# Kernel optimization log

Measured on AMD Instinct MI355X. Metric: run time of the kernel, lower is better.

The kernel has to match this reference:

```python
import jax, jax.numpy as jnp
import numpy as np


def _sobel_mag(x_bchw):
    # per-channel Sobel gradient magnitude, then mean over channels -> [B,1,H,W]
    B, C, H, W = x_bchw.shape
    kx = jnp.array([[-1, 0, 1], [-2, 0, 2], [-1, 0, 1]], dtype=x_bchw.dtype).reshape(1, 1, 3, 3)
    ky = jnp.array([[-1, -2, -1], [0, 0, 0], [1, 2, 1]], dtype=x_bchw.dtype).reshape(1, 1, 3, 3)
    xf = x_bchw.reshape(B * C, 1, H, W)
    dn = ('NCHW', 'OIHW', 'NCHW')
    gx = jax.lax.conv_general_dilated(xf, kx, (1, 1), 'SAME', dimension_numbers=dn)
    gy = jax.lax.conv_general_dilated(xf, ky, (1, 1), 'SAME', dimension_numbers=dn)
    mag = jnp.sqrt(gx * gx + gy * gy + 1e-8).reshape(B, C, H, W)
    return mag.mean(axis=1, keepdims=True)


def _bi_wkv(w, u, k, v):
    # Bidirectional WKV (Vision-RWKV):
    # y_t = (sum_{i!=t} exp(k_i - (|t-i|-1)*w) v_i + exp(u+k_t) v_t)
    #     / (sum_{i!=t} exp(k_i - (|t-i|-1)*w)     + exp(u+k_t))
    # w,u: [C];  k,v: [B,T,C]. Numerically stable prefix scans in both directions.
    B, T, C = k.shape
    kt = jnp.transpose(k, (1, 0, 2))  # [T,B,C]
    vt = jnp.transpose(v, (1, 0, 2))

    def scan_dir(ks, vs):
        def step(carry, kv):
            a, b, pp = carry  # running num, den at log-offset pp (exclusive prefix)
            kk, vv = kv
            out = (a, b, pp)
            ww = pp - w  # decay one step
            p = jnp.maximum(ww, kk)
            e1 = jnp.exp(ww - p)
            e2 = jnp.exp(kk - p)
            return (e1 * a + e2 * vv, e1 * b + e2, p), out
        init = (jnp.zeros((B, C), k.dtype), jnp.zeros((B, C), k.dtype),
                jnp.full((B, C), -1e38, k.dtype))
        _, (a, b, pp) = jax.lax.scan(step, init, (ks, vs))
        return a, b, pp

    af, bf, pf = scan_dir(kt, vt)                       # contributions i < t
    ab, bb, pb = scan_dir(kt[::-1], vt[::-1])           # contributions i > t
    ab, bb, pb = ab[::-1], bb[::-1], pb[::-1]

    ps = u + kt                                         # self term exponent
    m = jnp.maximum(jnp.maximum(pf, pb), ps)
    ef = jnp.exp(pf - m)
    eb = jnp.exp(pb - m)
    es = jnp.exp(ps - m)
    num = af * ef + ab * eb + es * vt
    den = bf * ef + bb * eb + es
    return jnp.transpose(num / den, (1, 0, 2))  # [B,T,C]


def setup_inputs() -> dict:
    key = jax.random.key(0)
    ks = jax.random.split(key, 8)
    B, H, W, C = 8, 64, 64, 256
    T = H * W
    s = 1.0 / np.sqrt(C)
    return {
        'x': jax.random.normal(ks[0], (B, T, C), jnp.float32),
        'Wk': jax.random.normal(ks[1], (C, C), jnp.float32) * s,
        'Wv': jax.random.normal(ks[2], (C, C), jnp.float32) * s,
        'Wr': jax.random.normal(ks[3], (C, C), jnp.float32) * s,
        'Wo': jax.random.normal(ks[4], (C, C), jnp.float32) * s,
        'spatial_decay': jax.random.uniform(ks[5], (C,), jnp.float32, 0.5, 1.5),
        'spatial_first': jax.random.uniform(ks[6], (C,), jnp.float32, 0.5, 1.5),
        'H': H,
        'W': W,
    }


def reference(x, Wk, Wv, Wr, Wo, spatial_decay, spatial_first, H, W):
    B, T, C = x.shape
    k = x @ Wk.T
    v = x @ Wv.T
    r = x @ Wr.T
    sr = jax.nn.sigmoid(r)
    # edge gate
    x_hw = jnp.transpose(x, (0, 2, 1)).reshape(B, C, H, W)
    edge_g = jax.nn.sigmoid(_sobel_mag(x_hw)).reshape(B, 1, T)
    sr = sr + jnp.transpose(edge_g, (0, 2, 1))
    # bi-directional WKV with w,u scaled by 1/T (as in forward)
    xwkv = _bi_wkv(spatial_decay / T, spatial_first / T, k, v)
    return (sr * xwkv) @ Wo.T
```

## Files before the change

### kernel.cpp

```cpp
#include <hip/hip_runtime.h>
#include <hip/hip_bf16.h>

#define TB 8
#define TT 4096
#define TC 256
#define NC2 128
#define CL2 32

#define K2 512
#define BM 128
#define BN 128
#define BK 64

typedef _Float16 half8 __attribute__((ext_vector_type(8)));
typedef _Float16 half2v __attribute__((ext_vector_type(2)));
typedef float floatx4 __attribute__((ext_vector_type(4)));

#define GLDS16(g, l) __builtin_amdgcn_global_load_lds( \
    (const __attribute__((address_space(1))) void*)(g), \
    (__attribute__((address_space(3))) void*)(l), 16, 0, 0)

__global__ __launch_bounds__(256) void sobconv(
    const float* __restrict__ x, _Float16* __restrict__ X2,
    float* __restrict__ edge)
{
    int t = blockIdx.x & (TT - 1);
    int b = blockIdx.x >> 12;
    int h = t >> 6, w = t & 63;
    int c = threadIdx.x;

    float n[3][3];
    #pragma unroll
    for (int dh = 0; dh < 3; dh++) {
        int hh = h + dh - 1;
        #pragma unroll
        for (int dw = 0; dw < 3; dw++) {
            int ww = w + dw - 1;
            float val = 0.f;
            if (hh >= 0 && hh < 64 && ww >= 0 && ww < 64)
                val = x[((size_t)(b * TT + (hh << 6) + ww)) * TC + c];
            n[dh][dw] = val;
        }
    }
    float xc = n[1][1];
    _Float16 hi = (_Float16)xc;
    _Float16 lo = (_Float16)(xc - (float)hi);
    half2v p; p.x = hi; p.y = lo;
    *(half2v*)(X2 + ((size_t)(b * TT + t)) * K2 + 2 * c) = p;

    float gx = (n[0][2] - n[0][0]) + 2.f * (n[1][2] - n[1][0]) + (n[2][2] - n[2][0]);
    float gy = (n[2][0] + 2.f * n[2][1] + n[2][2]) - (n[0][0] + 2.f * n[0][1] + n[0][2]);
    float mag = sqrtf(gx * gx + gy * gy + 1e-8f);

    #pragma unroll
    for (int off = 32; off > 0; off >>= 1) mag += __shfl_down(mag, off, 64);
    __shared__ float part[4];
    if ((threadIdx.x & 63) == 0) part[threadIdx.x >> 6] = mag;
    __syncthreads();
    if (threadIdx.x == 0) {
        float s = part[0] + part[1] + part[2] + part[3];
        edge[blockIdx.x] = 1.f / (1.f + __expf(-s * (1.f / 256.f)));
    }
}

__global__ __launch_bounds__(256) void convert_w(
    const float* __restrict__ Wk, const float* __restrict__ Wv,
    const float* __restrict__ Wr, const float* __restrict__ Wo,
    _Float16* __restrict__ W2, _Float16* __restrict__ Wo2)
{
    int t = blockIdx.x * 256 + threadIdx.x;
    int wsel = t >> 16;
    int i = t & 65535;
    const float* src = (wsel == 0) ? Wk : (wsel == 1) ? Wv : (wsel == 2) ? Wr : Wo;
    _Float16* dst = (wsel < 3) ? (W2 + (size_t)wsel * TC * K2) : Wo2;
    _Float16 h = (_Float16)src[i];
    half2v p; p.x = h; p.y = h;
    *(half2v*)(dst + 2 * (size_t)i) = p;
}

__global__ __launch_bounds__(256) void gemm_f16(
    const _Float16* __restrict__ A2,
    const _Float16* __restrict__ W0, const _Float16* __restrict__ W1,
    const _Float16* __restrict__ W2p,
    void* __restrict__ C0, void* __restrict__ C1, void* __restrict__ C2,
    int ops)
{
    __shared__ __align__(16) char smem[32768];
    _Float16* As = (_Float16*)smem;
    _Float16* Bs = (_Float16*)(smem + 16384);

    int by = blockIdx.y;
    int wsel = by >> 1;
    const _Float16* W = (wsel == 0) ? W0 : (wsel == 1) ? W1 : W2p;
    void* Cc          = (wsel == 0) ? C0 : (wsel == 1) ? C1 : C2;
    int col0 = (by & 1) * BN;
    int row0 = blockIdx.x * BM;
    int op = (ops >> (2 * wsel)) & 3;

    int tid = threadIdx.x;
    int lane = tid & 63;
    int wv = tid >> 6;
    int qm = (wv >> 1) * 64;
    int qn = (wv & 1) * 64;

    const _Float16* Ag = A2 + (size_t)row0 * K2;
    const _Float16* Bg = W + (size_t)col0 * K2;

    floatx4 acc[4][4];
    #pragma unroll
    for (int i = 0; i < 4; i++)
        #pragma unroll
        for (int j = 0; j < 4; j++)
            acc[i][j] = (floatx4){0.f, 0.f, 0.f, 0.f};

    for (int kb = 0; kb < K2; kb += BK) {
        __syncthreads();
        #pragma unroll
        for (int i = 0; i < 4; i++) {
            int seg = i * 256 + tid;
            int row = seg >> 3;
            int s = seg & 7;
            int sg = s ^ (row & 7);
            GLDS16(Ag + (size_t)row * K2 + kb + sg * 8, &As[seg * 8]);
            GLDS16(Bg + (size_t)row * K2 + kb + sg * 8, &Bs[seg * 8]);
        }
        __syncthreads();
        #pragma unroll
        for (int kk = 0; kk < 2; kk++) {
            int sl = kk * 4 + (lane >> 4);
            half8 a[4], b[4];
            #pragma unroll
            for (int i = 0; i < 4; i++) {
                int ra = qm + i * 16 + (lane & 15);
                a[i] = *(const half8*)&As[ra * BK + ((sl ^ (ra & 7)) * 8)];
                int rb = qn + i * 16 + (lane & 15);
                b[i] = *(const half8*)&Bs[rb * BK + ((sl ^ (rb & 7)) * 8)];
            }
            #pragma unroll
            for (int i = 0; i < 4; i++)
                #pragma unroll
                for (int j = 0; j < 4; j++)
                    acc[i][j] = __builtin_amdgcn_mfma_f32_16x16x32_f16(
                        a[i], b[j], acc[i][j], 0, 0, 0);
        }
    }

    int mr0 = (lane >> 4) * 4;
    int nc = lane & 15;
    if (op == 2) {
        __syncthreads();
        ushort* tile = (ushort*)smem;
        #pragma unroll
        for (int i = 0; i < 4; i++)
            #pragma unroll
            for (int r = 0; r < 4; r++) {
                int ml = qm + i * 16 + mr0 + r;
                #pragma unroll
                for (int j = 0; j < 4; j++) {
                    int nl = qn + j * 16 + nc;
                    float vv = __expf(acc[i][j][r]);
                    _Float16 hh = (_Float16)vv;
                    tile[ml * 128 + (nl ^ (((ml >> 2) & 3) << 4))] = *(ushort*)&hh;
                }
            }
        __syncthreads();
        _Float16* Ch = (_Float16*)Cc;
        #pragma unroll
        for (int k = 0; k < 8; k++) {
            int seg = k * 256 + tid;
            int tr = seg >> 4;
            int ts = seg & 15;
            int ts2 = ts ^ (((tr >> 2) & 3) << 1);
            float4 val = *(const float4*)&tile[tr * 128 + ts2 * 8];
            ((float4*)(Ch + (size_t)(row0 + tr) * TC + col0))[ts] = val;
        }
    } else {
        float* Cf = (float*)Cc;
        #pragma unroll
        for (int i = 0; i < 4; i++) {
            #pragma unroll
            for (int r = 0; r < 4; r++) {
                int m = row0 + qm + i * 16 + mr0 + r;
                float* crow = Cf + (size_t)m * TC + col0 + qn;
                #pragma unroll
                for (int j = 0; j < 4; j++) {
                    float vvv = acc[i][j][r];
                    if (op == 1) vvv = 1.f / (1.f + __expf(-vvv));
                    crow[j * 16 + nc] = vvv;
                }
            }
        }
    }
}

__global__ __launch_bounds__(256) void wkv_chunk_sums(
    const _Float16* __restrict__ ekp, const float* __restrict__ vp,
    const float* __restrict__ decay,
    float* __restrict__ SaF, float* __restrict__ SbF,
    float* __restrict__ RaB, float* __restrict__ RbB)
{
    int tid = blockIdx.x * 256 + threadIdx.x;
    int c = tid & 255;
    int j = (tid >> 8) & (NC2 - 1);
    int b = tid >> 15;
    float w = decay[c] * (1.f / (float)TT);
    float d = __expf(-w);
    size_t base = ((size_t)(b * TT + j * CL2)) * TC + c;
    float Sa = 0.f, Sb = 0.f, Ra = 0.f, Rb = 0.f, pw = 1.f;
    #pragma unroll
    for (int i = 0; i < CL2; i++) {
        float ek = (float)ekp[base + (size_t)i * TC];
        float vv = vp[base + (size_t)i * TC];
        float ekv = ek * vv;
        Sa = fmaf(d, Sa, ekv);
        Sb = fmaf(d, Sb, ek);
        Ra = fmaf(pw, ekv, Ra);
        Rb = fmaf(pw, ek, Rb);
        pw *= d;
    }
    int idx = (b * NC2 + j) * TC + c;
    SaF[idx] = Sa; SbF[idx] = Sb; RaB[idx] = Ra; RbB[idx] = Rb;
}

__global__ __launch_bounds__(256) void wkv_carries(
    const float* __restrict__ SaF, const float* __restrict__ SbF,
    const float* __restrict__ RaB, const float* __restrict__ RbB,
    const float* __restrict__ decay,
    float* __restrict__ CfA, float* __restrict__ CfB,
    float* __restrict__ CbA, float* __restrict__ CbB)
{
    int gw = (blockIdx.x * 256 + threadIdx.x) >> 6;
    int lane = threadIdx.x & 63;
    int c = gw & 255, b = gw >> 8;
    float w = decay[c] * (1.f / (float)TT);
    float D = __expf(-(float)CL2 * w);
    int base = b * NC2 * TC + c;
    int j0 = 2 * lane, j1 = 2 * lane + 1;
    int r0 = NC2 - 1 - j0, r1 = NC2 - 2 - j0;

    float sa0 = SaF[base + j0 * TC], sa1 = SaF[base + j1 * TC];
    float sb0 = SbF[base + j0 * TC], sb1 = SbF[base + j1 * TC];
    float qa0 = RaB[base + r0 * TC], qa1 = RaB[base + r1 * TC];
    float qb0 = RbB[base + r0 * TC], qb1 = RbB[base + r1 * TC];

    float pa = fmaf(D, sa0, sa1), pb = fmaf(D, sb0, sb1);
    float ra = fmaf(D, qa0, qa1), rb = fmaf(D, qb0, qb1);

    float dp = D * D;
    #pragma unroll
    for (int off = 1; off < 64; off <<= 1) {
        float ta = __shfl_up(pa, off, 64);
        float tb = __shfl_up(pb, off, 64);
        float ua = __shfl_up(ra, off, 64);
        float ub = __shfl_up(rb, off, 64);
        if (lane >= off) {
            pa = fmaf(dp, ta, pa); pb = fmaf(dp, tb, pb);
            ra = fmaf(dp, ua, ra); rb = fmaf(dp, ub, rb);
        }
        dp = dp * dp;
    }
    float ppa = __shfl_up(pa, 1, 64);
    float ppb = __shfl_up(pb, 1, 64);
    float pra = __shfl_up(ra, 1, 64);
    float prb = __shfl_up(rb, 1, 64);
    if (lane == 0) { ppa = 0.f; ppb = 0.f; pra = 0.f; prb = 0.f; }

    CfA[base + j0 * TC] = ppa;
    CfA[base + j1 * TC] = fmaf(D, ppa, sa0);
    CfB[base + j0 * TC] = ppb;
    CfB[base + j1 * TC] = fmaf(D, ppb, sb0);
    CbA[base + r0 * TC] = pra;
    CbA[base + r1 * TC] = fmaf(D, pra, qa0);
    CbB[base + r0 * TC] = prb;
    CbB[base + r1 * TC] = fmaf(D, prb, qb0);
}

__global__ __launch_bounds__(256) void wkv_combine(
    const _Float16* __restrict__ ekp, const float* __restrict__ vp,
    const float* __restrict__ srp, const float* __restrict__ edgep,
    const float* __restrict__ decay, const float* __restrict__ first,
    const float* __restrict__ CfA, const float* __restrict__ CfB,
    const float* __restrict__ CbA, const float* __restrict__ CbB,
    _Float16* __restrict__ Y2)
{
    int bid = blockIdx.x;
    int j = bid & (NC2 - 1);
    int b = bid >> 7;
    int c = threadIdx.x;

    float w = decay[c] * (1.f / (float)TT);
    float d = __expf(-w);
    float eu = __expf(first[c] * (1.f / (float)TT));
    int cidx = (b * NC2 + j) * TC + c;
    size_t base = ((size_t)(b * TT + j * CL2)) * TC + c;

    float abArr[CL2], bbArr[CL2];
    float ab = CbA[cidx], bb = CbB[cidx];
    #pragma unroll
    for (int i = CL2 - 1; i >= 0; i--) {
        float ek = (float)ekp[base + (size_t)i * TC];
        float vv = vp[base + (size_t)i * TC];
        abArr[i] = ab; bbArr[i] = bb;
        ab = fmaf(d, ab, ek * vv);
        bb = fmaf(d, bb, ek);
    }
    float af = CfA[cidx], bf = CfB[cidx];
    #pragma unroll
    for (int i = 0; i < CL2; i++) {
        size_t idx = base + (size_t)i * TC;
        float ek = (float)ekp[idx];
        float vv = vp[idx];
        float srv = srp[idx];
        float es = ek * eu;
        float num = af + abArr[i] + es * vv;
        float den = bf + bbArr[i] + es;
        float ev = edgep[b * TT + j * CL2 + i];
        float yv = (srv + ev) * (num / den);
        _Float16 yh = (_Float16)yv;
        _Float16 yl = (_Float16)(yv - (float)yh);
        half2v p; p.x = yh; p.y = yl;
        size_t m = (size_t)(b * TT + j * CL2 + i);
        *(half2v*)(Y2 + m * K2 + 2 * c) = p;
        af = fmaf(d, af, ek * vv);
        bf = fmaf(d, bf, ek);
    }
}

extern "C" void kernel_launch(void* const* d_in, const int* in_sizes, int n_in,
                              void* d_out, int out_size, void* d_ws, size_t ws_size,
                              hipStream_t stream)
{
    const float* x      = (const float*)d_in[0];
    const float* Wk     = (const float*)d_in[1];
    const float* Wv     = (const float*)d_in[2];
    const float* Wr     = (const float*)d_in[3];
    const float* Wo     = (const float*)d_in[4];
    const float* sdecay = (const float*)d_in[5];
    const float* sfirst = (const float*)d_in[6];
    float* out = (float*)d_out;

    char* ws = (char*)d_ws;
    size_t off = 0;
    const size_t MB32 = (size_t)TB * TT * TC * sizeof(float);
    const size_t XH   = (size_t)TB * TT * K2 * sizeof(_Float16);
    _Float16* X2   = (_Float16*)(ws + off); off += XH;
    _Float16* ekh  = (_Float16*)(ws + off); off += MB32 / 2;
    float* vbuf  = (float*)(ws + off); off += MB32;
    float* srbuf = (float*)(ws + off); off += MB32;
    _Float16* W2  = (_Float16*)(ws + off); off += (size_t)3 * TC * K2 * sizeof(_Float16);
    _Float16* Wo2 = (_Float16*)(ws + off); off += (size_t)TC * K2 * sizeof(_Float16);
    float* edge  = (float*)(ws + off); off += (size_t)TB * TT * sizeof(float);
    const size_t CHB = (size_t)TB * NC2 * TC * sizeof(float);
    float* SaF = (float*)(ws + off); off += CHB;
    float* SbF = (float*)(ws + off); off += CHB;
    float* RaB = (float*)(ws + off); off += CHB;
    float* RbB = (float*)(ws + off); off += CHB;
    float* CfA = (float*)(ws + off); off += CHB;
    float* CfB = (float*)(ws + off); off += CHB;
    float* CbA = (float*)(ws + off); off += CHB;
    float* CbB = (float*)(ws + off); off += CHB;

    const int MBLK = (TB * TT) / BM;

    convert_w<<<(4 * TC * TC) / 256, 256, 0, stream>>>(Wk, Wv, Wr, Wo, W2, Wo2);
    sobconv<<<TB * TT, 256, 0, stream>>>(x, X2, edge);

    int ops1 = (2 << 0) | (0 << 2) | (1 << 4);
    gemm_f16<<<dim3(MBLK, 6), 256, 0, stream>>>(
        X2, W2, W2 + (size_t)TC * K2, W2 + (size_t)2 * TC * K2,
        ekh, vbuf, srbuf, ops1);

    wkv_chunk_sums<<<(TB * NC2 * TC) / 256, 256, 0, stream>>>(
        ekh, vbuf, sdecay, SaF, SbF, RaB, RbB);
    wkv_carries<<<(TB * TC * 64) / 256, 256, 0, stream>>>(
        SaF, SbF, RaB, RbB, sdecay, CfA, CfB, CbA, CbB);
    wkv_combine<<<TB * NC2, 256, 0, stream>>>(
        ekh, vbuf, srbuf, edge, sdecay, sfirst, CfA, CfB, CbA, CbB, X2);

    gemm_f16<<<dim3(MBLK, 2), 256, 0, stream>>>(
        X2, Wo2, Wo2, Wo2, out, out, out, 0);
}
```

Measured before the change: 222.5 us.

## Split hi/lo activations into separate planes and widen GEMM tile to full N

Stores the fp16 hi and lo parts of activations in two separate arrays instead of interleaving them along a doubled K. The GEMM now loads the weight tile once and issues two MFMAs per (hi, lo) pair, with a 128x256 block tile (BK=32), which removes the duplicated weight storage and halves the B-operand traffic. The weight conversion is also folded into the Sobel prep kernel, saving a launch. The exp-to-fp16 epilogue now writes directly to global instead of staging through LDS, so its stores are less coalesced. The larger accumulator array raises register pressure.

```diff
diff --git a/kernel.cpp b/kernel.cpp
--- a/kernel.cpp
+++ b/kernel.cpp
@@ -7,23 +7,35 @@
 #define NC2 128
 #define CL2 32
 
-#define K2 512
-#define BM 128
-#define BN 128
-#define BK 64
-
 typedef _Float16 half8 __attribute__((ext_vector_type(8)));
-typedef _Float16 half2v __attribute__((ext_vector_type(2)));
+typedef _Float16 half4v __attribute__((ext_vector_type(4)));
 typedef float floatx4 __attribute__((ext_vector_type(4)));
 
 #define GLDS16(g, l) __builtin_amdgcn_global_load_lds( \
     (const __attribute__((address_space(1))) void*)(g), \
     (__attribute__((address_space(3))) void*)(l), 16, 0, 0)
 
-__global__ __launch_bounds__(256) void sobconv(
-    const float* __restrict__ x, _Float16* __restrict__ X2,
-    float* __restrict__ edge)
-{
+__global__ __launch_bounds__(256) void prep(
+    const float* __restrict__ x,
+    const float* __restrict__ Wk, const float* __restrict__ Wv,
+    const float* __restrict__ Wr, const float* __restrict__ Wo,
+    _Float16* __restrict__ Xh, _Float16* __restrict__ Xl,
+    _Float16* __restrict__ Wf, float* __restrict__ edge)
+{
+    if (blockIdx.x >= TB * TT) {
+        int t4 = (blockIdx.x - TB * TT) * 256 + threadIdx.x;
+        int f = t4 * 4;
+        int wsel = f >> 16;
+        int i = f & 65535;
+        const float* src = (wsel == 0) ? Wk : (wsel == 1) ? Wv :
+                           (wsel == 2) ? Wr : Wo;
+        float4 v = *(const float4*)(src + i);
+        half4v h;
+        h.x = (_Float16)v.x; h.y = (_Float16)v.y;
+        h.z = (_Float16)v.z; h.w = (_Float16)v.w;
+        *(half4v*)(Wf + (size_t)wsel * 65536 + i) = h;
+        return;
+    }
     int t = blockIdx.x & (TT - 1);
     int b = blockIdx.x >> 12;
     int h = t >> 6, w = t & 63;
@@ -45,8 +57,9 @@
     float xc = n[1][1];
     _Float16 hi = (_Float16)xc;
     _Float16 lo = (_Float16)(xc - (float)hi);
-    half2v p; p.x = hi; p.y = lo;
-    *(half2v*)(X2 + ((size_t)(b * TT + t)) * K2 + 2 * c) = p;
+    size_t mi = (size_t)(b * TT + t) * TC + c;
+    Xh[mi] = hi;
+    Xl[mi] = lo;
 
     float gx = (n[0][2] - n[0][0]) + 2.f * (n[1][2] - n[1][0]) + (n[2][2] - n[2][0]);
     float gy = (n[2][0] + 2.f * n[2][1] + n[2][2]) - (n[0][0] + 2.f * n[0][1] + n[0][2]);
@@ -63,131 +76,106 @@
     }
 }
 
-__global__ __launch_bounds__(256) void convert_w(
-    const float* __restrict__ Wk, const float* __restrict__ Wv,
-    const float* __restrict__ Wr, const float* __restrict__ Wo,
-    _Float16* __restrict__ W2, _Float16* __restrict__ Wo2)
-{
-    int t = blockIdx.x * 256 + threadIdx.x;
-    int wsel = t >> 16;
-    int i = t & 65535;
-    const float* src = (wsel == 0) ? Wk : (wsel == 1) ? Wv : (wsel == 2) ? Wr : Wo;
-    _Float16* dst = (wsel < 3) ? (W2 + (size_t)wsel * TC * K2) : Wo2;
-    _Float16 h = (_Float16)src[i];
-    half2v p; p.x = h; p.y = h;
-    *(half2v*)(dst + 2 * (size_t)i) = p;
-}
-
-__global__ __launch_bounds__(256) void gemm_f16(
-    const _Float16* __restrict__ A2,
+__global__ __launch_bounds__(256, 2) void gemm_split(
+    const _Float16* __restrict__ Ah_g, const _Float16* __restrict__ Al_g,
     const _Float16* __restrict__ W0, const _Float16* __restrict__ W1,
     const _Float16* __restrict__ W2p,
     void* __restrict__ C0, void* __restrict__ C1, void* __restrict__ C2,
     int ops)
 {
-    __shared__ __align__(16) char smem[32768];
-    _Float16* As = (_Float16*)smem;
-    _Float16* Bs = (_Float16*)(smem + 16384);
-
-    int by = blockIdx.y;
-    int wsel = by >> 1;
+    __shared__ __align__(16) _Float16 smem[16384];
+    _Float16* Ah = smem;
+    _Float16* Al = smem + 4096;
+    _Float16* Bs = smem + 8192;
+
+    int wsel = blockIdx.y;
     const _Float16* W = (wsel == 0) ? W0 : (wsel == 1) ? W1 : W2p;
     void* Cc          = (wsel == 0) ? C0 : (wsel == 1) ? C1 : C2;
-    int col0 = (by & 1) * BN;
-    int row0 = blockIdx.x * BM;
     int op = (ops >> (2 * wsel)) & 3;
+    int row0 = blockIdx.x * 128;
 
     int tid = threadIdx.x;
     int lane = tid & 63;
     int wv = tid >> 6;
     int qm = (wv >> 1) * 64;
-    int qn = (wv & 1) * 64;
-
-    const _Float16* Ag = A2 + (size_t)row0 * K2;
-    const _Float16* Bg = W + (size_t)col0 * K2;
-
-    floatx4 acc[4][4];
+    int qn = (wv & 1) * 128;
+
+    floatx4 acc[4][8];
     #pragma unroll
     for (int i = 0; i < 4; i++)
         #pragma unroll
-        for (int j = 0; j < 4; j++)
+        for (int j = 0; j < 8; j++)
             acc[i][j] = (floatx4){0.f, 0.f, 0.f, 0.f};
 
-    for (int kb = 0; kb < K2; kb += BK) {
+    for (int kb = 0; kb < 256; kb += 32) {
         __syncthreads();
         #pragma unroll
+        for (int r = 0; r < 2; r++) {
+            int q = r * 256 + tid;
+            int row = q >> 2;
+            int s = q & 3;
+            int g = (s - row - (row >> 2)) & 3;
+            size_t goff = (size_t)(row0 + row) * TC + kb + g * 8;
+            GLDS16(Ah_g + goff, &Ah[q * 8]);
+            GLDS16(Al_g + goff, &Al[q * 8]);
+        }
+        #pragma unroll
+        for (int r = 0; r < 4; r++) {
+            int q = r * 256 + tid;
+            int row = q >> 2;
+            int s = q & 3;
+            int g = (s - row - (row >> 2)) & 3;
+            GLDS16(W + (size_t)row * TC + kb + g * 8, &Bs[q * 8]);
+        }
+        __syncthreads();
+        int sl = lane >> 4;
+        half8 ah[4], al[4], b[8];
+        #pragma unroll
         for (int i = 0; i < 4; i++) {
-            int seg = i * 256 + tid;
-            int row = seg >> 3;
-            int s = seg & 7;
-            int sg = s ^ (row & 7);
-            GLDS16(Ag + (size_t)row * K2 + kb + sg * 8, &As[seg * 8]);
-            GLDS16(Bg + (size_t)row * K2 + kb + sg * 8, &Bs[seg * 8]);
-        }
-        __syncthreads();
-        #pragma unroll
-        for (int kk = 0; kk < 2; kk++) {
-            int sl = kk * 4 + (lane >> 4);
-            half8 a[4], b[4];
+            int ra = qm + i * 16 + (lane & 15);
+            int sa = (sl + ra + (ra >> 2)) & 3;
+            ah[i] = *(const half8*)&Ah[ra * 32 + sa * 8];
+            al[i] = *(const half8*)&Al[ra * 32 + sa * 8];
+        }
+        #pragma unroll
+        for (int j = 0; j < 8; j++) {
+            int rb = qn + j * 16 + (lane & 15);
+            int sb = (sl + rb + (rb >> 2)) & 3;
+            b[j] = *(const half8*)&Bs[rb * 32 + sb * 8];
+        }
+        #pragma unroll
+        for (int i = 0; i < 4; i++)
             #pragma unroll
-            for (int i = 0; i < 4; i++) {
-                int ra = qm + i * 16 + (lane & 15);
-                a[i] = *(const half8*)&As[ra * BK + ((sl ^ (ra & 7)) * 8)];
-                int rb = qn + i * 16 + (lane & 15);
-                b[i] = *(const half8*)&Bs[rb * BK + ((sl ^ (rb & 7)) * 8)];
+            for (int j = 0; j < 8; j++) {
+                acc[i][j] = __builtin_amdgcn_mfma_f32_16x16x32_f16(
+                    ah[i], b[j], acc[i][j], 0, 0, 0);
+                acc[i][j] = __builtin_amdgcn_mfma_f32_16x16x32_f16(
+                    al[i], b[j], acc[i][j], 0, 0, 0);
             }
-            #pragma unroll
-            for (int i = 0; i < 4; i++)
-                #pragma unroll
-                for (int j = 0; j < 4; j++)
-                    acc[i][j] = __builtin_amdgcn_mfma_f32_16x16x32_f16(
-                        a[i], b[j], acc[i][j], 0, 0, 0);
-        }
     }
 
     int mr0 = (lane >> 4) * 4;
     int nc = lane & 15;
-    if (op == 2) {
-        __syncthreads();
-        ushort* tile = (ushort*)smem;
-        #pragma unroll
-        for (int i = 0; i < 4; i++)
-            #pragma unroll
-            for (int r = 0; r < 4; r++) {
-                int ml = qm + i * 16 + mr0 + r;
+    #pragma unroll
+    for (int i = 0; i < 4; i++) {
+        #pragma unroll
+        for (int r = 0; r < 4; r++) {
+            int m = row0 + qm + i * 16 + mr0 + r;
+            if (op == 2) {
+                _Float16* crow = (_Float16*)Cc + (size_t)m * TC + qn + nc;
                 #pragma unroll
-                for (int j = 0; j < 4; j++) {
-                    int nl = qn + j * 16 + nc;
-                    float vv = __expf(acc[i][j][r]);
-                    _Float16 hh = (_Float16)vv;
-                    tile[ml * 128 + (nl ^ (((ml >> 2) & 3) << 4))] = *(ushort*)&hh;
-                }
-            }
-        __syncthreads();
-        _Float16* Ch = (_Float16*)Cc;
-        #pragma unroll
-        for (int k = 0; k < 8; k++) {
-            int seg = k * 256 + tid;
-            int tr = seg >> 4;
-            int ts = seg & 15;
-            int ts2 = ts ^ (((tr >> 2) & 3) << 1);
-            float4 val = *(const float4*)&tile[tr * 128 + ts2 * 8];
-            ((float4*)(Ch + (size_t)(row0 + tr) * TC + col0))[ts] = val;
-        }
-    } else {
-        float* Cf = (float*)Cc;
-        #pragma unroll
-        for (int i = 0; i < 4; i++) {
-            #pragma unroll
-            for (int r = 0; r < 4; r++) {
-                int m = row0 + qm + i * 16 + mr0 + r;
-                float* crow = Cf + (size_t)m * TC + col0 + qn;
+                for (int j = 0; j < 8; j++)
+                    crow[j * 16] = (_Float16)__expf(acc[i][j][r]);
+            } else if (op == 1) {
+                float* crow = (float*)Cc + (size_t)m * TC + qn + nc;
                 #pragma unroll
-                for (int j = 0; j < 4; j++) {
-                    float vvv = acc[i][j][r];
-                    if (op == 1) vvv = 1.f / (1.f + __expf(-vvv));
-                    crow[j * 16 + nc] = vvv;
-                }
+                for (int j = 0; j < 8; j++)
+                    crow[j * 16] = 1.f / (1.f + __expf(-acc[i][j][r]));
+            } else {
+                float* crow = (float*)Cc + (size_t)m * TC + qn + nc;
+                #pragma unroll
+                for (int j = 0; j < 8; j++)
+                    crow[j * 16] = acc[i][j][r];
             }
         }
     }
@@ -281,7 +269,7 @@
     const float* __restrict__ decay, const float* __restrict__ first,
     const float* __restrict__ CfA, const float* __restrict__ CfB,
     const float* __restrict__ CbA, const float* __restrict__ CbB,
-    _Float16* __restrict__ Y2)
+    _Float16* __restrict__ Yh, _Float16* __restrict__ Yl)
 {
     int bid = blockIdx.x;
     int j = bid & (NC2 - 1);
@@ -318,9 +306,8 @@
         float yv = (srv + ev) * (num / den);
         _Float16 yh = (_Float16)yv;
         _Float16 yl = (_Float16)(yv - (float)yh);
-        half2v p; p.x = yh; p.y = yl;
-        size_t m = (size_t)(b * TT + j * CL2 + i);
-        *(half2v*)(Y2 + m * K2 + 2 * c) = p;
+        Yh[idx] = yh;
+        Yl[idx] = yl;
         af = fmaf(d, af, ek * vv);
         bf = fmaf(d, bf, ek);
     }
@@ -341,14 +328,13 @@
 
     char* ws = (char*)d_ws;
     size_t off = 0;
-    const size_t MB32 = (size_t)TB * TT * TC * sizeof(float);
-    const size_t XH   = (size_t)TB * TT * K2 * sizeof(_Float16);
-    _Float16* X2   = (_Float16*)(ws + off); off += XH;
-    _Float16* ekh  = (_Float16*)(ws + off); off += MB32 / 2;
-    float* vbuf  = (float*)(ws + off); off += MB32;
-    float* srbuf = (float*)(ws + off); off += MB32;
-    _Float16* W2  = (_Float16*)(ws + off); off += (size_t)3 * TC * K2 * sizeof(_Float16);
-    _Float16* Wo2 = (_Float16*)(ws + off); off += (size_t)TC * K2 * sizeof(_Float16);
+    const size_t PH = (size_t)TB * TT * TC * sizeof(_Float16);
+    _Float16* Xh  = (_Float16*)(ws + off); off += PH;
+    _Float16* Xl  = (_Float16*)(ws + off); off += PH;
+    _Float16* ekh = (_Float16*)(ws + off); off += PH;
+    float* vbuf  = (float*)(ws + off); off += 2 * PH;
+    float* srbuf = (float*)(ws + off); off += 2 * PH;
+    _Float16* Wf = (_Float16*)(ws + off); off += (size_t)4 * TC * TC * sizeof(_Float16);
     float* edge  = (float*)(ws + off); off += (size_t)TB * TT * sizeof(float);
     const size_t CHB = (size_t)TB * NC2 * TC * sizeof(float);
     float* SaF = (float*)(ws + off); off += CHB;
@@ -360,23 +346,24 @@
     float* CbA = (float*)(ws + off); off += CHB;
     float* CbB = (float*)(ws + off); off += CHB;
 
-    const int MBLK = (TB * TT) / BM;
-
-    convert_w<<<(4 * TC * TC) / 256, 256, 0, stream>>>(Wk, Wv, Wr, Wo, W2, Wo2);
-    sobconv<<<TB * TT, 256, 0, stream>>>(x, X2, edge);
-
-    int ops1 = (2 << 0) | (0 << 2) | (1 << 4);
-    gemm_f16<<<dim3(MBLK, 6), 256, 0, stream>>>(
-        X2, W2, W2 + (size_t)TC * K2, W2 + (size_t)2 * TC * K2,
-        ekh, vbuf, srbuf, ops1);
+    _Float16* WfK = Wf;
+    _Float16* WfV = Wf + (size_t)TC * TC;
+    _Float16* WfR = Wf + (size_t)2 * TC * TC;
+    _Float16* WfO = Wf + (size_t)3 * TC * TC;
+
+    prep<<<TB * TT + 256, 256, 0, stream>>>(x, Wk, Wv, Wr, Wo, Xh, Xl, Wf, edge);
+
+    int ops1 = 2 | (0 << 2) | (1 << 4);
+    gemm_split<<<dim3((TB * TT) / 128, 3), 256, 0, stream>>>(
+        Xh, Xl, WfK, WfV, WfR, ekh, vbuf, srbuf, ops1);
 
     wkv_chunk_sums<<<(TB * NC2 * TC) / 256, 256, 0, stream>>>(
         ekh, vbuf, sdecay, SaF, SbF, RaB, RbB);
     wkv_carries<<<(TB * TC * 64) / 256, 256, 0, stream>>>(
         SaF, SbF, RaB, RbB, sdecay, CfA, CfB, CbA, CbB);
     wkv_combine<<<TB * NC2, 256, 0, stream>>>(
-        ekh, vbuf, srbuf, edge, sdecay, sfirst, CfA, CfB, CbA, CbB, X2);
-
-    gemm_f16<<<dim3(MBLK, 2), 256, 0, stream>>>(
-        X2, Wo2, Wo2, Wo2, out, out, out, 0);
-}
+        ekh, vbuf, srbuf, edge, sdecay, sfirst, CfA, CfB, CbA, CbB, Xh, Xl);
+
+    gemm_split<<<dim3((TB * TT) / 128, 1), 256, 0, stream>>>(
+        Xh, Xl, WfO, WfO, WfO, out, out, out, 0);
+}
```

Result: no change. 219.3 us (-1.5%).
